# Kernel tuning notes

Hardware: AMD Instinct MI355X
Metric: run time of the kernel (lower is better)

The kernel has to match this reference:

```python
import jax, jax.numpy as jnp
import numpy as np

B, D_IN, H0, H1, LAT, C = 8192, 2048, 1024, 512, 128, 8
SCALE = 0.02  # weight init scale to keep activations well-conditioned


def _unshared_linear_relu(x, labels, W, b):
    """Per-cluster Linear+ReLU routing. x:[B,din], W:[C,din,dout], b:[C,dout].
    Computes all cluster branches then selects per-row branch (same math as
    torch's mask gather->Linear->scatter; rows never reorder)."""
    y = jax.nn.relu(jnp.einsum('bi,cio->bco', x, W) + b[None, :, :])  # [B,C,dout]
    return jnp.take_along_axis(y, labels[:, None, None], axis=1)[:, 0, :]


def setup_inputs() -> dict:
    key = jax.random.key(0)
    ks = jax.random.split(key, 12)
    return {
        'x': jax.random.normal(ks[0], (B, D_IN), dtype=jnp.float32),
        'cluster_labels': jax.random.randint(ks[1], (B,), 0, C, dtype=jnp.int32),
        'eps': jax.random.normal(ks[2], (B, LAT), dtype=jnp.float32),
        'W_enc0': jax.random.normal(ks[3], (C, D_IN, H0), dtype=jnp.float32) * SCALE,
        'b_enc0': jnp.zeros((C, H0), dtype=jnp.float32),
        'W_enc1': jax.random.normal(ks[4], (H0, H1), dtype=jnp.float32) * SCALE,
        'b_enc1': jnp.zeros((H1,), dtype=jnp.float32),
        'W_mu': jax.random.normal(ks[5], (H1, LAT), dtype=jnp.float32) * SCALE,
        'b_mu': jnp.zeros((LAT,), dtype=jnp.float32),
        'W_logvar': jax.random.normal(ks[6], (H1, LAT), dtype=jnp.float32) * SCALE,
        'b_logvar': jnp.zeros((LAT,), dtype=jnp.float32),
        'W_dec0': jax.random.normal(ks[7], (LAT, H1), dtype=jnp.float32) * SCALE,
        'b_dec0': jnp.zeros((H1,), dtype=jnp.float32),
        'W_dec1': jax.random.normal(ks[8], (C, H1, H0), dtype=jnp.float32) * SCALE,
        'b_dec1': jnp.zeros((C, H0), dtype=jnp.float32),
        'W_out': jax.random.normal(ks[9], (H0, D_IN), dtype=jnp.float32) * SCALE,
        'b_out': jnp.zeros((D_IN,), dtype=jnp.float32),
    }


def reference(x, cluster_labels, eps,
              W_enc0, b_enc0, W_enc1, b_enc1,
              W_mu, b_mu, W_logvar, b_logvar,
              W_dec0, b_dec0, W_dec1, b_dec1,
              W_out, b_out):
    labels = cluster_labels.astype(jnp.int32)
    # encoder: unshared layer 0, shared layer 1
    h = _unshared_linear_relu(x, labels, W_enc0, b_enc0)          # [B, H0]
    h = jax.nn.relu(h @ W_enc1 + b_enc1)                          # [B, H1]
    # shared latent heads
    mu = h @ W_mu + b_mu                                          # [B, LAT]
    logvar = h @ W_logvar + b_logvar                              # [B, LAT]
    # reparameterize
    z = mu + eps * jnp.exp(0.5 * logvar)                          # [B, LAT]
    # decoder: shared layer 0, unshared layer 1 (hidden_dims reversed)
    d = jax.nn.relu(z @ W_dec0 + b_dec0)                          # [B, H1]
    d = _unshared_linear_relu(d, labels, W_dec1, b_dec1)          # [B, H0]
    # shared output layer (no activation)
    recon = d @ W_out + b_out                                     # [B, D_IN]
    return recon, mu, logvar
```

## Files before the change

### kernel.cpp

```cpp
#include <hip/hip_runtime.h>


#define DEVI __device__ __forceinline__

constexpr int B_    = 8192;
constexpr int DIN   = 2048;
constexpr int H0_   = 1024;
constexpr int H1_   = 512;
constexpr int LAT_  = 128;
constexpr int NC    = 8;

constexpr int BM = 128, BN = 128, BK = 32;
constexpr int TCAP   = 72;
constexpr int BP_CAP = TCAP * BM;

#define MI_NTILES 8
#define MI_TILEC  16

typedef __attribute__((ext_vector_type(8))) short bf16x8;
typedef __attribute__((ext_vector_type(4))) float f32x4;

#define LDS_BARRIER() asm volatile("s_waitcnt lgkmcnt(0)\n\ts_barrier" ::: "memory")

DEVI unsigned short f2bf(float f) {
  union { float f; unsigned u; } a; a.f = f;
  unsigned r = a.u + 0x7fffu + ((a.u >> 16) & 1u);
  return (unsigned short)(r >> 16);
}

constexpr size_t AL256(size_t x) { return (x + 255) & ~(size_t)255; }
constexpr size_t OFF_META = 0;
constexpr size_t OFF_PERM = 512;
constexpr size_t OFF_XG   = AL256(OFF_PERM + (size_t)BP_CAP * 4);
constexpr size_t OFF_H0   = AL256(OFF_XG  + (size_t)BP_CAP * DIN * 2);
constexpr size_t OFF_H1   = AL256(OFF_H0  + (size_t)BP_CAP * H0_ * 2);
constexpr size_t OFF_MLP  = AL256(OFF_H1  + (size_t)BP_CAP * H1_ * 2);
constexpr size_t OFF_BML  = AL256(OFF_MLP + (size_t)BP_CAP * 256 * 4);
constexpr size_t OFF_WT0  = AL256(OFF_BML + 256 * 4);
constexpr size_t OFF_WT1  = AL256(OFF_WT0 + (size_t)NC * DIN * H0_ * 2);
constexpr size_t OFF_WML  = AL256(OFF_WT1 + (size_t)H0_ * H1_ * 2);
constexpr size_t OFF_WD0  = AL256(OFF_WML + (size_t)256 * H1_ * 2);
constexpr size_t OFF_WD1  = AL256(OFF_WD0 + (size_t)LAT_ * H1_ * 2);
constexpr size_t OFF_WOUT = AL256(OFF_WD1 + (size_t)NC * H1_ * H0_ * 2);

__global__ void setup_all(const int* __restrict__ labels, int* __restrict__ meta,
                          int* __restrict__ perm, const float* __restrict__ b_mu,
                          const float* __restrict__ b_lv, float* __restrict__ b_ml) {
  __shared__ int cnt[NC], base[NC];
  int t = threadIdx.x;
  if (t < NC) cnt[t] = 0;
  if (t < 256) b_ml[t] = (t < 128) ? b_mu[t] : b_lv[t - 128];
  __syncthreads();
  for (int i = t; i < B_; i += 1024) atomicAdd(&cnt[labels[i]], 1);
  for (int i = t; i < BP_CAP; i += 1024) perm[i] = -1;
  __syncthreads();
  if (t == 0) {
    int off = 0, nt = 0;
    for (int c = 0; c < NC; ++c) {
      base[c] = off;
      int k = (cnt[c] + BM - 1) >> 7;
      for (int j = 0; j < k; ++j) meta[MI_TILEC + nt + j] = c;
      nt += k;
      off += k << 7;
    }
    meta[MI_NTILES] = nt;
  }
  __syncthreads();
  if (t < NC) cnt[t] = base[t];
  __syncthreads();
  for (int i = t; i < B_; i += 1024) {
    int pos = atomicAdd(&cnt[labels[i]], 1);
    perm[pos] = i;
  }
}

struct SegDesc { const float* src; unsigned short* dst; int K, N, nb, tstart; };
struct SegTable { SegDesc s[7]; };

__global__ void convert_all(SegTable t) {
  __shared__ float tl[64][33];
  int tile = blockIdx.x;
  int si = 0;
#pragma unroll
  for (int i = 1; i < 7; ++i) si += (tile >= t.s[i].tstart) ? 1 : 0;
  const SegDesc sd = t.s[si];
  int local = tile - sd.tstart;
  int tpb = (sd.K >> 6) * (sd.N >> 5);
  int b = local / tpb, rem = local - b * tpb;
  int tk = rem / (sd.N >> 5), tn = rem - tk * (sd.N >> 5);
  const float* s = sd.src + (size_t)b * sd.K * sd.N;
  unsigned short* d = sd.dst + (size_t)b * sd.K * sd.N;
  int n0 = tn * 32, k0 = tk * 64;
  int tx = threadIdx.x, ty = threadIdx.y;
  for (int i = ty; i < 64; i += 8)
    tl[i][tx] = s[(size_t)(k0 + i) * sd.N + n0 + tx];
  __syncthreads();
  int id = ty * 32 + tx;
  int j = id >> 3;
  int kk = (id & 7) * 8;
  unsigned short v[8];
#pragma unroll
  for (int q = 0; q < 8; ++q) v[q] = f2bf(tl[kk + q][j]);
  *(int4*)&d[(size_t)(n0 + j) * sd.K + k0 + kk] = *(int4*)v;
}

__global__ void gather_x_kernel(const float* __restrict__ x, const int* __restrict__ perm,
                                unsigned short* __restrict__ xg) {
  int p = blockIdx.x;
  int c4 = blockIdx.y * 256 + threadIdx.x;
  int src = perm[p];
  float4 v = make_float4(0.f, 0.f, 0.f, 0.f);
  if (src >= 0) v = ((const float4*)(x + (size_t)src * DIN))[c4];
  ushort4 o;
  o.x = f2bf(v.x); o.y = f2bf(v.y); o.z = f2bf(v.z); o.w = f2bf(v.w);
  ((ushort4*)(xg + (size_t)p * DIN))[c4] = o;
}

__global__ void z_kernel(const float* __restrict__ mlp, const float* __restrict__ eps,
                         const int* __restrict__ perm, unsigned short* __restrict__ z,
                         float* __restrict__ out_mu, float* __restrict__ out_lv) {
  int p = blockIdx.x, j = threadIdx.x;
  int src = perm[p];
  float zz = 0.f;
  if (src >= 0) {
    float m = mlp[(size_t)p * 256 + j];
    float l = mlp[(size_t)p * 256 + 128 + j];
    zz = m + eps[(size_t)src * LAT_ + j] * expf(0.5f * l);
    out_mu[(size_t)src * LAT_ + j] = m;
    out_lv[(size_t)src * LAT_ + j] = l;
  }
  z[(size_t)p * LAT_ + j] = f2bf(zz);
}

template <int OUT_MODE, bool RELU, bool PCW, bool PCB>
__global__ __launch_bounds__(256, 2)
void gemm_kernel(const unsigned short* __restrict__ A,
                 const unsigned short* __restrict__ Bt,
                 const float* __restrict__ bias,
                 void* __restrict__ Cout,
                 const int* __restrict__ meta,
                 const int* __restrict__ perm,
                 int K, int N, int ldc) {
  const int ntn = N >> 7;
  const int sup = 8 * ntn;
  const int gid = blockIdx.x;
  const int tm  = (gid / sup) * 8 + (gid & 7);
  const int tn  = (gid % sup) >> 3;
  if (tm >= meta[MI_NTILES]) return;

  int cluster = 0;
  if (PCW || PCB) cluster = meta[MI_TILEC + tm];
  const unsigned short* Bp = Bt + (PCW ? (size_t)cluster * (size_t)N * K : 0);
  const float* bb = bias + (PCB ? (size_t)cluster * N : 0);

  __shared__ alignas(16) unsigned short As[2][BM * BK];
  __shared__ alignas(16) unsigned short Bs[2][BN * BK];

  const int tid  = threadIdx.x;
  const int w    = tid >> 6, lane = tid & 63;
  const int fr   = lane & 15, quad = lane >> 4;
  const int wm   = (w >> 1) * 64, wn = (w & 1) * 64;

  const int s0 = (w * 2 + 0) * 64 + lane;
  const int s1 = (w * 2 + 1) * 64 + lane;
  const int r0 = s0 >> 2, r1 = s1 >> 2;
  const int c0 = (s0 & 3) ^ ((r0 >> 1) & 3);
  const int c1 = (s1 & 3) ^ ((r1 >> 1) & 3);
  const unsigned short* pa0 = A  + (size_t)(tm * BM + r0) * K + c0 * 8;
  const unsigned short* pa1 = A  + (size_t)(tm * BM + r1) * K + c1 * 8;
  const unsigned short* pb0 = Bp + (size_t)(tn * BN + r0) * K + c0 * 8;
  const unsigned short* pb1 = Bp + (size_t)(tn * BN + r1) * K + c1 * 8;
  const int l0 = s0 * 8, l1 = s1 * 8;

  int aro[4], bro[4];
#pragma unroll
  for (int i = 0; i < 4; ++i) {
    int R = wm + i * 16 + fr;
    aro[i] = (R * 4 + (quad ^ ((R >> 1) & 3))) * 8;
    R = wn + i * 16 + fr;
    bro[i] = (R * 4 + (quad ^ ((R >> 1) & 3))) * 8;
  }

  f32x4 acc[4][4] = {};

  auto compute = [&](int buf) {
    bf16x8 af[4], bfr[4];
#pragma unroll
    for (int i = 0; i < 4; ++i) af[i]  = *(const bf16x8*)&As[buf][aro[i]];
#pragma unroll
    for (int i = 0; i < 4; ++i) bfr[i] = *(const bf16x8*)&Bs[buf][bro[i]];
#pragma unroll
    for (int mi = 0; mi < 4; ++mi)
#pragma unroll
      for (int ni = 0; ni < 4; ++ni)
        acc[mi][ni] = __builtin_amdgcn_mfma_f32_16x16x32_bf16(af[mi], bfr[ni], acc[mi][ni], 0, 0, 0);
  };

  const int nt = K / BK;

  int4 a0A, a0B, b0A, b0B;
  int4 a1A, a1B, b1A, b1B;

  a0A = *(const int4*)(pa0);  a0B = *(const int4*)(pa1);
  b0A = *(const int4*)(pb0);  b0B = *(const int4*)(pb1);
  a1A = *(const int4*)(pa0 + BK);  a1B = *(const int4*)(pa1 + BK);
  b1A = *(const int4*)(pb0 + BK);  b1B = *(const int4*)(pb1 + BK);
  *(int4*)&As[0][l0] = a0A;  *(int4*)&As[0][l1] = a0B;
  *(int4*)&Bs[0][l0] = b0A;  *(int4*)&Bs[0][l1] = b0B;
  a0A = *(const int4*)(pa0 + 2 * BK);  a0B = *(const int4*)(pa1 + 2 * BK);
  b0A = *(const int4*)(pb0 + 2 * BK);  b0B = *(const int4*)(pb1 + 2 * BK);
  LDS_BARRIER();

  compute(0);
  *(int4*)&As[1][l0] = a1A;  *(int4*)&As[1][l1] = a1B;
  *(int4*)&Bs[1][l0] = b1A;  *(int4*)&Bs[1][l1] = b1B;
  if (3 < nt) {
    a1A = *(const int4*)(pa0 + 3 * BK);  a1B = *(const int4*)(pa1 + 3 * BK);
    b1A = *(const int4*)(pb0 + 3 * BK);  b1B = *(const int4*)(pb1 + 3 * BK);
  }
  LDS_BARRIER();

  for (int j = 1; j + 2 < nt; j += 2) {
    compute(1);
    *(int4*)&As[0][l0] = a0A;  *(int4*)&As[0][l1] = a0B;
    *(int4*)&Bs[0][l0] = b0A;  *(int4*)&Bs[0][l1] = b0B;
    if (j + 3 < nt) {
      int k = (j + 3) * BK;
      a0A = *(const int4*)(pa0 + k);  a0B = *(const int4*)(pa1 + k);
      b0A = *(const int4*)(pb0 + k);  b0B = *(const int4*)(pb1 + k);
    }
    LDS_BARRIER();
    compute(0);
    *(int4*)&As[1][l0] = a1A;  *(int4*)&As[1][l1] = a1B;
    *(int4*)&Bs[1][l0] = b1A;  *(int4*)&Bs[1][l1] = b1B;
    if (j + 4 < nt) {
      int k = (j + 4) * BK;
      a1A = *(const int4*)(pa0 + k);  a1B = *(const int4*)(pa1 + k);
      b1A = *(const int4*)(pb0 + k);  b1B = *(const int4*)(pb1 + k);
    }
    LDS_BARRIER();
  }

  compute(1);

  float bv[4];
#pragma unroll
  for (int ni = 0; ni < 4; ++ni) bv[ni] = bb[tn * BN + wn + ni * 16 + fr];

#pragma unroll
  for (int mi = 0; mi < 4; ++mi) {
#pragma unroll
    for (int r = 0; r < 4; ++r) {
      int m = tm * BM + wm + mi * 16 + quad * 4 + r;
      int orow = m;
      if (OUT_MODE == 2) orow = perm[m];
#pragma unroll
      for (int ni = 0; ni < 4; ++ni) {
        int n = tn * BN + wn + ni * 16 + fr;
        float v = acc[mi][ni][r] + bv[ni];
        if (RELU) v = fmaxf(v, 0.f);
        if (OUT_MODE == 0) {
          ((unsigned short*)Cout)[(size_t)m * N + n] = f2bf(v);
        } else if (OUT_MODE == 1) {
          ((float*)Cout)[(size_t)m * N + n] = v;
        } else {
          if (orow >= 0) ((float*)Cout)[(size_t)orow * ldc + n] = v;
        }
      }
    }
  }
}

extern "C" void kernel_launch(void* const* d_in, const int* in_sizes, int n_in,
                              void* d_out, int out_size, void* d_ws, size_t ws_size,
                              hipStream_t stream) {
  const float* x        = (const float*)d_in[0];
  const int*   labels   = (const int*)d_in[1];
  const float* eps      = (const float*)d_in[2];
  const float* W_enc0   = (const float*)d_in[3];
  const float* b_enc0   = (const float*)d_in[4];
  const float* W_enc1   = (const float*)d_in[5];
  const float* b_enc1   = (const float*)d_in[6];
  const float* W_mu     = (const float*)d_in[7];
  const float* b_mu     = (const float*)d_in[8];
  const float* W_logvar = (const float*)d_in[9];
  const float* b_logvar = (const float*)d_in[10];
  const float* W_dec0   = (const float*)d_in[11];
  const float* b_dec0   = (const float*)d_in[12];
  const float* W_dec1   = (const float*)d_in[13];
  const float* b_dec1   = (const float*)d_in[14];
  const float* W_out    = (const float*)d_in[15];
  const float* b_out    = (const float*)d_in[16];

  float* out_recon = (float*)d_out;
  float* out_mu    = out_recon + (size_t)B_ * DIN;
  float* out_lv    = out_mu + (size_t)B_ * LAT_;

  char* ws = (char*)d_ws;
  int* meta            = (int*)(ws + OFF_META);
  int* perm            = (int*)(ws + OFF_PERM);
  unsigned short* xg   = (unsigned short*)(ws + OFF_XG);
  unsigned short* h0   = (unsigned short*)(ws + OFF_H0);
  unsigned short* h1   = (unsigned short*)(ws + OFF_H1);
  float* mlp           = (float*)(ws + OFF_MLP);
  float* b_ml          = (float*)(ws + OFF_BML);
  unsigned short* Wt0  = (unsigned short*)(ws + OFF_WT0);
  unsigned short* Wt1  = (unsigned short*)(ws + OFF_WT1);
  unsigned short* Wml  = (unsigned short*)(ws + OFF_WML);
  unsigned short* Wd0  = (unsigned short*)(ws + OFF_WD0);
  unsigned short* Wd1  = (unsigned short*)(ws + OFF_WD1);
  unsigned short* Wout = (unsigned short*)(ws + OFF_WOUT);
  unsigned short* d1 = xg;
  unsigned short* d0 = h0;
  unsigned short* z  = h1;

  SegTable st;
  int ts = 0;
  auto seg = [&](int i, const float* s, unsigned short* d, int K, int N, int nb) {
    st.s[i] = SegDesc{s, d, K, N, nb, ts};
    ts += (K / 64) * (N / 32) * nb;
  };
  seg(0, W_enc0,   Wt0,                      DIN,  H0_,  NC);
  seg(1, W_enc1,   Wt1,                      H0_,  H1_,  1);
  seg(2, W_mu,     Wml,                      H1_,  LAT_, 1);
  seg(3, W_logvar, Wml + (size_t)LAT_ * H1_, H1_,  LAT_, 1);
  seg(4, W_dec0,   Wd0,                      LAT_, H1_,  1);
  seg(5, W_dec1,   Wd1,                      H1_,  H0_,  NC);
  seg(6, W_out,    Wout,                     H0_,  DIN,  1);

  setup_all<<<1, 1024, 0, stream>>>(labels, meta, perm, b_mu, b_logvar, b_ml);
  convert_all<<<ts, dim3(32, 8), 0, stream>>>(st);
  gather_x_kernel<<<dim3(BP_CAP, DIN / (256 * 4)), 256, 0, stream>>>(x, perm, xg);

  gemm_kernel<0, true, true, true><<<TCAP * (H0_ / BN), 256, 0, stream>>>(
      xg, Wt0, b_enc0, h0, meta, perm, DIN, H0_, 0);
  gemm_kernel<0, true, false, false><<<TCAP * (H1_ / BN), 256, 0, stream>>>(
      h0, Wt1, b_enc1, h1, meta, perm, H0_, H1_, 0);
  gemm_kernel<1, false, false, false><<<TCAP * (256 / BN), 256, 0, stream>>>(
      h1, Wml, b_ml, mlp, meta, perm, H1_, 256, 0);
  z_kernel<<<BP_CAP, 128, 0, stream>>>(mlp, eps, perm, z, out_mu, out_lv);
  gemm_kernel<0, true, false, false><<<TCAP * (H1_ / BN), 256, 0, stream>>>(
      z, Wd0, b_dec0, d0, meta, perm, LAT_, H1_, 0);
  gemm_kernel<0, true, true, true><<<TCAP * (H0_ / BN), 256, 0, stream>>>(
      d0, Wd1, b_dec1, d1, meta, perm, H1_, H0_, 0);
  gemm_kernel<2, false, false, false><<<TCAP * (DIN / BN), 256, 0, stream>>>(
      d1, Wout, b_out, out_recon, meta, perm, H0_, DIN, DIN);

  (void)in_sizes; (void)n_in; (void)out_size; (void)ws_size;
}
```

Before: 421.2 us.

## Use direct global-to-LDS loads with a triple-buffered GEMM pipeline

```diff
diff --git a/kernel.cpp b/kernel.cpp
--- a/kernel.cpp
+++ b/kernel.cpp
@@ -20,12 +20,19 @@
 typedef __attribute__((ext_vector_type(8))) short bf16x8;
 typedef __attribute__((ext_vector_type(4))) float f32x4;
 
-#define LDS_BARRIER() asm volatile("s_waitcnt lgkmcnt(0)\n\ts_barrier" ::: "memory")
+#define VMBAR(N) asm volatile("s_waitcnt vmcnt(" #N ") lgkmcnt(0)\n\ts_barrier" ::: "memory")
 
 DEVI unsigned short f2bf(float f) {
   union { float f; unsigned u; } a; a.f = f;
   unsigned r = a.u + 0x7fffu + ((a.u >> 16) & 1u);
   return (unsigned short)(r >> 16);
+}
+
+DEVI void glds16(const unsigned short* g, unsigned short* l) {
+  __builtin_amdgcn_global_load_lds(
+      (const __attribute__((address_space(1))) unsigned int*)g,
+      (__attribute__((address_space(3))) unsigned int*)l,
+      16, 0, 0);
 }
 
 constexpr size_t AL256(size_t x) { return (x + 255) & ~(size_t)255; }
@@ -153,24 +160,25 @@
   const unsigned short* Bp = Bt + (PCW ? (size_t)cluster * (size_t)N * K : 0);
   const float* bb = bias + (PCB ? (size_t)cluster * N : 0);
 
-  __shared__ alignas(16) unsigned short As[2][BM * BK];
-  __shared__ alignas(16) unsigned short Bs[2][BN * BK];
+  __shared__ alignas(16) unsigned short As[3][BM * BK];
+  __shared__ alignas(16) unsigned short Bs[3][BN * BK];
 
   const int tid  = threadIdx.x;
   const int w    = tid >> 6, lane = tid & 63;
   const int fr   = lane & 15, quad = lane >> 4;
   const int wm   = (w >> 1) * 64, wn = (w & 1) * 64;
 
-  const int s0 = (w * 2 + 0) * 64 + lane;
-  const int s1 = (w * 2 + 1) * 64 + lane;
-  const int r0 = s0 >> 2, r1 = s1 >> 2;
-  const int c0 = (s0 & 3) ^ ((r0 >> 1) & 3);
-  const int c1 = (s1 & 3) ^ ((r1 >> 1) & 3);
-  const unsigned short* pa0 = A  + (size_t)(tm * BM + r0) * K + c0 * 8;
-  const unsigned short* pa1 = A  + (size_t)(tm * BM + r1) * K + c1 * 8;
-  const unsigned short* pb0 = Bp + (size_t)(tn * BN + r0) * K + c0 * 8;
-  const unsigned short* pb1 = Bp + (size_t)(tn * BN + r1) * K + c1 * 8;
-  const int l0 = s0 * 8, l1 = s1 * 8;
+  const int sU = (w * 2 + 0) * 64 + lane;
+  const int sV = (w * 2 + 1) * 64 + lane;
+  const int rU = sU >> 2, rV = sV >> 2;
+  const int cU = (sU & 3) ^ ((rU >> 1) & 3);
+  const int cV = (sV & 3) ^ ((rV >> 1) & 3);
+  const unsigned short* paU = A  + (size_t)(tm * BM + rU) * K + cU * 8;
+  const unsigned short* paV = A  + (size_t)(tm * BM + rV) * K + cV * 8;
+  const unsigned short* pbU = Bp + (size_t)(tn * BN + rU) * K + cU * 8;
+  const unsigned short* pbV = Bp + (size_t)(tn * BN + rV) * K + cV * 8;
+  const int ldU = (w * 2 + 0) * 512;
+  const int ldV = (w * 2 + 1) * 512;
 
   int aro[4], bro[4];
 #pragma unroll
@@ -183,6 +191,13 @@
 
   f32x4 acc[4][4] = {};
 
+  auto stage = [&](int buf, int k0) {
+    glds16(paU + k0, &As[buf][ldU]);
+    glds16(paV + k0, &As[buf][ldV]);
+    glds16(pbU + k0, &Bs[buf][ldU]);
+    glds16(pbV + k0, &Bs[buf][ldV]);
+  };
+
   auto compute = [&](int buf) {
     bf16x8 af[4], bfr[4];
 #pragma unroll
@@ -198,50 +213,21 @@
 
   const int nt = K / BK;
 
-  int4 a0A, a0B, b0A, b0B;
-  int4 a1A, a1B, b1A, b1B;
-
-  a0A = *(const int4*)(pa0);  a0B = *(const int4*)(pa1);
-  b0A = *(const int4*)(pb0);  b0B = *(const int4*)(pb1);
-  a1A = *(const int4*)(pa0 + BK);  a1B = *(const int4*)(pa1 + BK);
-  b1A = *(const int4*)(pb0 + BK);  b1B = *(const int4*)(pb1 + BK);
-  *(int4*)&As[0][l0] = a0A;  *(int4*)&As[0][l1] = a0B;
-  *(int4*)&Bs[0][l0] = b0A;  *(int4*)&Bs[0][l1] = b0B;
-  a0A = *(const int4*)(pa0 + 2 * BK);  a0B = *(const int4*)(pa1 + 2 * BK);
-  b0A = *(const int4*)(pb0 + 2 * BK);  b0B = *(const int4*)(pb1 + 2 * BK);
-  LDS_BARRIER();
-
-  compute(0);
-  *(int4*)&As[1][l0] = a1A;  *(int4*)&As[1][l1] = a1B;
-  *(int4*)&Bs[1][l0] = b1A;  *(int4*)&Bs[1][l1] = b1B;
-  if (3 < nt) {
-    a1A = *(const int4*)(pa0 + 3 * BK);  a1B = *(const int4*)(pa1 + 3 * BK);
-    b1A = *(const int4*)(pb0 + 3 * BK);  b1B = *(const int4*)(pb1 + 3 * BK);
-  }
-  LDS_BARRIER();
-
-  for (int j = 1; j + 2 < nt; j += 2) {
-    compute(1);
-    *(int4*)&As[0][l0] = a0A;  *(int4*)&As[0][l1] = a0B;
-    *(int4*)&Bs[0][l0] = b0A;  *(int4*)&Bs[0][l1] = b0B;
-    if (j + 3 < nt) {
-      int k = (j + 3) * BK;
-      a0A = *(const int4*)(pa0 + k);  a0B = *(const int4*)(pa1 + k);
-      b0A = *(const int4*)(pb0 + k);  b0B = *(const int4*)(pb1 + k);
+  stage(0, 0);
+  stage(1, BK);
+  VMBAR(4);
+
+  int cur = 0;
+  for (int i = 0; i < nt; ++i) {
+    if (i + 2 < nt) {
+      int b2 = cur + 2; if (b2 >= 3) b2 -= 3;
+      stage(b2, (i + 2) * BK);
     }
-    LDS_BARRIER();
-    compute(0);
-    *(int4*)&As[1][l0] = a1A;  *(int4*)&As[1][l1] = a1B;
-    *(int4*)&Bs[1][l0] = b1A;  *(int4*)&Bs[1][l1] = b1B;
-    if (j + 4 < nt) {
-      int k = (j + 4) * BK;
-      a1A = *(const int4*)(pa0 + k);  a1B = *(const int4*)(pa1 + k);
-      b1A = *(const int4*)(pb0 + k);  b1B = *(const int4*)(pb1 + k);
-    }
-    LDS_BARRIER();
-  }
-
-  compute(1);
+    compute(cur);
+    if (i + 2 < nt)      VMBAR(4);
+    else if (i + 1 < nt) VMBAR(0);
+    ++cur; if (cur == 3) cur = 0;
+  }
 
   float bv[4];
 #pragma unroll
```

Result: slower. 438.7 us (+4.2%).
